# Performance work log

Measured on AMD Instinct MI355X. Metric: run time of the kernel, lower is better.

The kernel has to match this reference:

```python
import jax, jax.numpy as jnp
import numpy as np

TEMPERATURE = 0.07
KNN_AUG = True
NUM_NEIGHBORS = 10
B, N, D = 2048, 65536, 128
NUM_CLUSTERS = 100
EPS = 1e-12


def _l2_normalize(x):
    # matches torch F.normalize(dim=1): x / max(||x||, eps)
    norm = jnp.sqrt(jnp.sum(x * x, axis=1, keepdims=True))
    return x / jnp.maximum(norm, EPS)


def setup_inputs() -> dict:
    key = jax.random.key(0)
    k1, k2, k3, k4 = jax.random.split(key, 4)
    return {
        "features": jax.random.normal(k1, (B, D), dtype=jnp.float32),
        "cluster_idxes": jax.random.randint(k2, (B,), 0, NUM_CLUSTERS),
        "global_features": jax.random.normal(k3, (N, D), dtype=jnp.float32),
        "global_clusters": jax.random.randint(k4, (N,), 0, NUM_CLUSTERS),
    }


def reference(features, cluster_idxes, global_features, global_clusters):
    f = _l2_normalize(features)            # [B, D]
    g = _l2_normalize(global_features)     # [N, D]
    sim = (f @ g.T) / TEMPERATURE          # [B, N]

    # cluster-membership positive mask: [B, N]
    pos_mask = (cluster_idxes[:, None] == global_clusters[None, :]).astype(sim.dtype)

    if KNN_AUG:
        k_val = min(NUM_NEIGHBORS, sim.shape[-1])
        _, knn_idx = jax.lax.top_k(sim, k_val)  # [B, k]
        rows = jnp.arange(sim.shape[0])[:, None]
        knn_mask = jnp.zeros_like(pos_mask).at[rows, knn_idx].set(1.0)
        pos_mask = ((pos_mask + knn_mask) > 0).astype(sim.dtype)

    # masked log-softmax reduction (same math as original: exp/sum/log)
    log_prob = sim - jnp.log(jnp.sum(jnp.exp(sim), axis=1, keepdims=True) + EPS)  # [B, N]
    mean_log_prob_pos = jnp.sum(pos_mask * log_prob, axis=1) / (jnp.sum(pos_mask, axis=1) + EPS)
    return -jnp.mean(mean_log_prob_pos)
```

## Files before the change

### kernel.cpp

```cpp
#include <hip/hip_runtime.h>

#define B_ROWS 2048
#define N_GLB  65536
#define DDIM   128
#define NCLUST 100
#define INV_T  (1.0f/0.07f)
#define LOG2E  1.4426950408889634f
#define LN2    0.6931471805599453f
#define NSPLIT 16
#define CHUNK_COLS (N_GLB/NSPLIT)
#define ITERS (CHUNK_COLS/64)
#define ROWSB 16
#define GRPB 2048
#define TOPK 10
#define CAP  256
#define NSLICE 8
#define TAU_L2E (3.7881f*LOG2E)
#define CSC    65536.0f
#define INV_CSC (1.0f/65536.0f)
#define ZWORDS 105472

typedef __attribute__((ext_vector_type(4))) float f32x4;
typedef __attribute__((ext_vector_type(2))) long lg2;
typedef unsigned long long u64;

__device__ __forceinline__ unsigned fmono(float v) {
  unsigned u = __float_as_uint(v);
  return ((int)u < 0) ? ~u : (u | 0x80000000u);
}
__device__ __forceinline__ float fmono_inv(unsigned m) {
  unsigned u = (m & 0x80000000u) ? (m & 0x7FFFFFFFu) : ~m;
  return __uint_as_float(u);
}
__device__ __forceinline__ u64 mkkey(float val, int col) {
  return ((u64)fmono(val) << 32) | (unsigned)(~(unsigned)col);
}
__device__ __forceinline__ u64 umax64(u64 a, u64 b) { return a > b ? a : b; }

__device__ __forceinline__ float fp8d(unsigned b) {
  unsigned e = (b >> 3) & 15, m = b & 7;
  float v = e ? __uint_as_float(((e + 120u) << 23) | (m << 20))
              : (float)m * 0.001953125f;
  return (b & 0x80u) ? -v : v;
}

__global__ __launch_bounds__(256) void prep_kernel(
    const float* __restrict__ f, const float* __restrict__ g,
    char* __restrict__ wsf2, char* __restrict__ wsg2,
    float* __restrict__ inv_fT, float* __restrict__ inv_g,
    unsigned* __restrict__ zbase) {
  __shared__ unsigned short lds[1024];
  const int t = threadIdx.x, lane = t & 63, w = t >> 6;
  const int grp = blockIdx.x;
  const bool isf = grp < (B_ROWS / 16);

  if (isf) {
    int gid = grp * 256 + t;
    #pragma unroll
    for (int k = 0; k < 4; ++k) {
      int idx = gid + k * 32768;
      if (idx < ZWORDS) zbase[idx] = 0u;
    }
  }

  #pragma unroll
  for (int j = 0; j < 4; ++j) {
    int rit = w * 4 + j;
    int row = grp * 16 + rit;
    int rr = isf ? row : row - B_ROWS;
    const float* src = (isf ? f : g) + (size_t)rr * DDIM;
    float2 v = ((const float2*)src)[lane];
    float ss = v.x * v.x + v.y * v.y;
    #pragma unroll
    for (int m = 32; m; m >>= 1) ss += __shfl_xor(ss, m);
    float inv = 1.0f / fmaxf(sqrtf(ss), 1e-12f);
    if (lane == 0) { if (isf) inv_fT[rr] = inv * INV_T; else inv_g[rr] = inv; }
    float sc = isf ? inv * (INV_T * LOG2E) : inv;
    unsigned pk = __builtin_amdgcn_cvt_pk_fp8_f32(v.x * sc, v.y * sc, 0u, false);
    int k = 2 * lane;
    int off = ((k >> 6) << 10) + (((k >> 3) & 3) << 8) + (rit << 4)
            + (((k >> 5) & 1) << 3) + (k & 7);
    lds[off >> 1] = (unsigned short)(pk & 0xFFFFu);
  }
  __syncthreads();
  char* dst = isf ? (wsf2 + (size_t)grp * GRPB)
                  : (wsg2 + (size_t)(grp - B_ROWS / 16) * GRPB);
  ((uint2*)dst)[t] = ((const uint2*)lds)[t];
}

__global__ __launch_bounds__(256) void csum2_kernel(
    const float* __restrict__ g, const int* __restrict__ gclust,
    const float* __restrict__ inv_g,
    int* __restrict__ csum_i32, int* __restrict__ hist8) {
  __shared__ int cs[NCLUST * DDIM];
  __shared__ int hcnt[NCLUST];
  const int t = threadIdx.x, lane = t & 63, w = t >> 6;
  for (int i = t; i < NCLUST * DDIM; i += 256) cs[i] = 0;
  if (t < NCLUST) hcnt[t] = 0;
  __syncthreads();

  const int rbase = blockIdx.x * 256;
  const int rg = lane >> 4;
  const int ch = lane & 15;
  for (int step = 0; step < 16; ++step) {
    int row = rbase + step * 16 + w * 4 + rg;
    int c = gclust[row];
    float scale = inv_g[row] * CSC;
    const float* gp = g + (size_t)row * DDIM + 8 * ch;
    float4 a = *(const float4*)gp;
    float4 b = *(const float4*)(gp + 4);
    int* dst = &cs[c * DDIM + ch * 8];
    atomicAdd(dst + 0, (int)rintf(a.x * scale));
    atomicAdd(dst + 1, (int)rintf(a.y * scale));
    atomicAdd(dst + 2, (int)rintf(a.z * scale));
    atomicAdd(dst + 3, (int)rintf(a.w * scale));
    atomicAdd(dst + 4, (int)rintf(b.x * scale));
    atomicAdd(dst + 5, (int)rintf(b.y * scale));
    atomicAdd(dst + 6, (int)rintf(b.z * scale));
    atomicAdd(dst + 7, (int)rintf(b.w * scale));
    if (ch == 0) atomicAdd(&hcnt[c], 1);
  }
  __syncthreads();
  const int slice = blockIdx.x & (NSLICE - 1);
  for (int i = t; i < NCLUST * DDIM; i += 256) {
    int x = cs[i];
    if (x) atomicAdd(&csum_i32[(size_t)slice * NCLUST * DDIM + i], x);
  }
  if (t < NCLUST && hcnt[t]) atomicAdd(&hist8[slice * 128 + t], hcnt[t]);
}

#define PUSHQ(av, q)                                                            \
  if ((av) > TAU_L2E) {                                                         \
    int rw = r0 + lhi * 4 + (q);                                                \
    int slot = atomicAdd(&cnt[rw], 1);                                          \
    if (slot < CAP) { lv[rw * CAP + slot] = (av) * LN2; li[rw * CAP + slot] = colv; } \
  }

#define LOADB(dst, gptr)                                                        \
  { dst[0] = *(const uint4*)((gptr) + (size_t)lane * 16);                       \
    dst[1] = *(const uint4*)((gptr) + 1024 + (size_t)lane * 16); }

#define COMPUTE_REFILL(bb, itv, refbase, dorefill)                              \
  {                                                                             \
    f32x4 acA = {0,0,0,0}, acB = {0,0,0,0};                                     \
    lg2 bs0 = __builtin_bit_cast(lg2, bb[0]);                                   \
    lg2 bs1 = __builtin_bit_cast(lg2, bb[1]);                                   \
    if (dorefill) {                                                             \
      bb[0] = *(const uint4*)((refbase) + (size_t)lane * 16);                   \
      bb[1] = *(const uint4*)((refbase) + 1024 + (size_t)lane * 16);            \
    }                                                                           \
    acA = __builtin_amdgcn_mfma_f32_16x16x32_fp8_fp8(afr[0][0], bs0[0], acA, 0, 0, 0); \
    acB = __builtin_amdgcn_mfma_f32_16x16x32_fp8_fp8(afr[1][0], bs1[0], acB, 0, 0, 0); \
    acA = __builtin_amdgcn_mfma_f32_16x16x32_fp8_fp8(afr[0][1], bs0[1], acA, 0, 0, 0); \
    acB = __builtin_amdgcn_mfma_f32_16x16x32_fp8_fp8(afr[1][1], bs1[1], acB, 0, 0, 0); \
    f32x4 a = acA + acB;                                                        \
    se.x += __builtin_amdgcn_exp2f(a.x);                                        \
    se.y += __builtin_amdgcn_exp2f(a.y);                                        \
    se.z += __builtin_amdgcn_exp2f(a.z);                                        \
    se.w += __builtin_amdgcn_exp2f(a.w);                                        \
    float mx = fmaxf(fmaxf(a.x, a.y), fmaxf(a.z, a.w));                         \
    if (mx > TAU_L2E) {                                                         \
      const int colv = chunk * CHUNK_COLS + (itv) * 64 + w * 16 + l15;          \
      PUSHQ(a.x, 0) PUSHQ(a.y, 1) PUSHQ(a.z, 2) PUSHQ(a.w, 3)                   \
    }                                                                           \
  }

__global__ __launch_bounds__(256, 8) void sim_kernel(
    const char* __restrict__ wsf2, const char* __restrict__ wsg2,
    float* __restrict__ p_se, float* __restrict__ lv, int* __restrict__ li,
    int* __restrict__ cnt) {
  __shared__ float sered[4][ROWSB];
  const int t = threadIdx.x, lane = t & 63, w = t >> 6;
  const int l15 = lane & 15, lhi = lane >> 4;
  const int chunk = blockIdx.x;
  const int r0 = blockIdx.y * ROWSB;

  const char* fbase = wsf2 + (size_t)(r0 >> 4) * GRPB;
  lg2 afr[2];
  #pragma unroll
  for (int sp = 0; sp < 2; ++sp)
    afr[sp] = __builtin_bit_cast(lg2,
      *(const uint4*)(fbase + sp * 1024 + (size_t)lane * 16));

  f32x4 se = {0.f, 0.f, 0.f, 0.f};

  const char* gb = wsg2 + (size_t)(chunk * (CHUNK_COLS / 16) + w) * GRPB;
  uint4 b0[2], b1[2];
  LOADB(b0, gb)
  LOADB(b1, gb + 8192)
  for (int it = 0; it < ITERS; it += 2) {
    COMPUTE_REFILL(b0, it,     gb + 2 * 8192, it + 2 < ITERS)
    COMPUTE_REFILL(b1, it + 1, gb + 3 * 8192, it + 3 < ITERS)
    gb += 2 * 8192;
  }

  #pragma unroll
  for (int q = 0; q < 4; ++q) {
    float s = se[q];
    s += __shfl_xor(s, 1); s += __shfl_xor(s, 2);
    s += __shfl_xor(s, 4); s += __shfl_xor(s, 8);
    if (l15 == 0) sered[w][lhi * 4 + q] = s;
  }
  __syncthreads();
  if (t < ROWSB) {
    float s = sered[0][t] + sered[1][t] + sered[2][t] + sered[3][t];
    p_se[(size_t)(r0 + t) * NSPLIT + chunk] = s;
  }
}

__global__ __launch_bounds__(256) void merge_kernel(
    const float* __restrict__ f, const int* __restrict__ fclust,
    const int* __restrict__ gclust, const float* __restrict__ inv_fT,
    const float* __restrict__ p_se, const int* __restrict__ csum_i32,
    const int* __restrict__ hist8, const float* __restrict__ lv,
    const int* __restrict__ li, const int* __restrict__ cnt,
    const char* __restrict__ wsf2, const char* __restrict__ wsg2,
    float* __restrict__ rowv) {
  const int lane = threadIdx.x & 63, w = threadIdx.x >> 6;
  const int r = blockIdx.x * 4 + w;

  float sev = (lane < NSPLIT) ? p_se[(size_t)r * NSPLIT + lane] : 0.f;
  sev += __shfl_xor(sev, 8); sev += __shfl_xor(sev, 4);
  sev += __shfl_xor(sev, 2); sev += __shfl_xor(sev, 1);
  sev = __shfl(sev, 0);

  int rc = fclust[r];
  float2 fv = ((const float2*)(f + (size_t)r * DDIM))[lane];
  float sc = inv_fT[r];
  int ia = 0, ib = 0, hc = 0;
  #pragma unroll
  for (int s = 0; s < NSLICE; ++s) {
    ia += csum_i32[(size_t)s * NCLUST * DDIM + rc * DDIM + 2 * lane];
    ib += csum_i32[(size_t)s * NCLUST * DDIM + rc * DDIM + 2 * lane + 1];
    hc += hist8[s * 128 + rc];
  }
  float dt = fv.x * sc * (ia * INV_CSC) + fv.y * sc * (ib * INV_CSC);
  #pragma unroll
  for (int m = 32; m; m >>= 1) dt += __shfl_xor(dt, m);
  dt = __shfl(dt, 0);

  float Cc = (float)hc;
  int n = cnt[r];
  bool bad = (n < TOPK) || (n > CAP);
  float S10 = 0.f, C10 = 0.f;
  if (!bad) {
    u64 k0 = 0, k1 = 0, k2 = 0, k3 = 0;
    int e = lane;
    if (e < n) k0 = mkkey(lv[(size_t)r * CAP + e], li[(size_t)r * CAP + e]);
    e = lane + 64;
    if (e < n) k1 = mkkey(lv[(size_t)r * CAP + e], li[(size_t)r * CAP + e]);
    e = lane + 128;
    if (e < n) k2 = mkkey(lv[(size_t)r * CAP + e], li[(size_t)r * CAP + e]);
    e = lane + 192;
    if (e < n) k3 = mkkey(lv[(size_t)r * CAP + e], li[(size_t)r * CAP + e]);
    for (int it = 0; it < TOPK; ++it) {
      u64 best = umax64(umax64(k0, k1), umax64(k2, k3));
      #pragma unroll
      for (int m = 32; m; m >>= 1) best = umax64(best, __shfl_xor(best, m));
      float val = fmono_inv((unsigned)(best >> 32));
      int col = (int)(~(unsigned)(best & 0xFFFFFFFFull));
      int gc = gclust[col];
      if (gc != rc) { S10 += val; C10 += 1.f; }
      if (k0 == best) k0 = 0;
      if (k1 == best) k1 = 0;
      if (k2 == best) k2 = 0;
      if (k3 == best) k3 = 0;
    }
  } else {
    uint4 fr[8];
    #pragma unroll
    for (int pc = 0; pc < 8; ++pc)
      fr[pc] = *(const uint4*)(wsf2 + (size_t)(r >> 4) * GRPB + (pc >> 2) * 1024
                               + (pc & 3) * 256 + (r & 15) * 16);
    u64 tk[TOPK];
    #pragma unroll
    for (int i = 0; i < TOPK; ++i) tk[i] = 0;
    for (int col = lane; col < N_GLB; col += 64) {
      const char* gp = wsg2 + (size_t)(col >> 4) * GRPB + (col & 15) * 16;
      float acc = 0.f;
      #pragma unroll
      for (int pc = 0; pc < 8; ++pc) {
        uint4 gv = *(const uint4*)(gp + (pc >> 2) * 1024 + (pc & 3) * 256);
        uint4 fc = fr[pc];
        #pragma unroll
        for (int wd = 0; wd < 4; ++wd) {
          unsigned fa = (&fc.x)[wd], ga = (&gv.x)[wd];
          #pragma unroll
          for (int b = 0; b < 4; ++b)
            acc += fp8d((fa >> (8 * b)) & 0xFFu) * fp8d((ga >> (8 * b)) & 0xFFu);
        }
      }
      u64 key = mkkey(acc, col);
      if (key > tk[0]) {
        u64 cur = key;
        #pragma unroll
        for (int i = 0; i < TOPK - 1; ++i) {
          u64 nxt = tk[i + 1];
          u64 lo = cur < nxt ? cur : nxt;
          u64 hi = cur < nxt ? nxt : cur;
          tk[i] = lo; cur = hi;
        }
        tk[TOPK - 1] = cur;
      }
    }
    for (int it = 0; it < TOPK; ++it) {
      u64 best = tk[TOPK - 1];
      #pragma unroll
      for (int m = 32; m; m >>= 1) best = umax64(best, __shfl_xor(best, m));
      float val = fmono_inv((unsigned)(best >> 32)) * LN2;
      int col = (int)(~(unsigned)(best & 0xFFFFFFFFull));
      if (gclust[col] != rc) { S10 += val; C10 += 1.f; }
      if (tk[TOPK - 1] == best) {
        #pragma unroll
        for (int i = TOPK - 1; i > 0; --i) tk[i] = tk[i - 1];
        tk[0] = 0;
      }
    }
  }
  if (lane == 0) {
    float L = logf(sev + 1e-12f);
    float C = Cc + C10;
    rowv[r] = (dt + S10 - C * L) / (C + 1e-12f);
  }
}

__global__ void final_kernel(const float* __restrict__ rowv, float* __restrict__ out) {
  __shared__ float sm[256];
  int t = threadIdx.x;
  float s = 0.f;
  for (int i = t; i < B_ROWS; i += 256) s += rowv[i];
  sm[t] = s;
  __syncthreads();
  for (int o = 128; o; o >>= 1) { if (t < o) sm[t] += sm[t + o]; __syncthreads(); }
  if (t == 0) out[0] = -(sm[0] / (float)B_ROWS);
}

extern "C" void kernel_launch(void* const* d_in, const int* in_sizes, int n_in,
                              void* d_out, int out_size, void* d_ws, size_t ws_size,
                              hipStream_t stream) {
  const float* f  = (const float*)d_in[0];
  const int*   fc = (const int*)  d_in[1];
  const float* g  = (const float*)d_in[2];
  const int*   gc = (const int*)  d_in[3];
  float* out = (float*)d_out;

  char* ws = (char*)d_ws;
  char*  wsf2    = ws;
  char*  wsg2    = ws + 262144;
  float* inv_fT  = (float*)(ws + 8650752);
  float* inv_g   = (float*)(ws + 8658944);
  float* p_se    = (float*)(ws + 8921088);
  int*   csum_i32= (int*)  (ws + 9052160);
  int*   hist8   = (int*)  (ws + 9461760);
  int*   cnt     = (int*)  (ws + 9465856);
  unsigned* zbase= (unsigned*)(ws + 9052160);
  float* lv      = (float*)(ws + 9474048);
  int*   li      = (int*)  (ws + 11571200);
  float* rowv    = (float*)(ws + 13668352);

  prep_kernel<<<(B_ROWS + N_GLB) / 16, 256, 0, stream>>>(f, g, wsf2, wsg2,
                                                         inv_fT, inv_g, zbase);

  csum2_kernel<<<N_GLB / 256, 256, 0, stream>>>(g, gc, inv_g, csum_i32, hist8);

  dim3 grid(NSPLIT, B_ROWS / ROWSB);
  sim_kernel<<<grid, 256, 0, stream>>>(wsf2, wsg2, p_se, lv, li, cnt);

  merge_kernel<<<B_ROWS / 4, 256, 0, stream>>>(f, fc, gc, inv_fT, p_se, csum_i32,
                                               hist8, lv, li, cnt, wsf2, wsg2, rowv);
  final_kernel<<<1, 256, 0, stream>>>(rowv, out);
}
```

Measured before the change: 106.3 us.

## Fuse global-feature normalization and fp8 packing into cluster-sum kernel

The global-feature normalization and fp8 packing move out of the combined prep kernel into the cluster-sum kernel. The 32 MB g tensor is now read once instead of twice, and the inv_g buffer round-trip goes away. Blocks now cover 128 rows instead of 256, which doubles the block count, and the cluster-sum slices go from 8 to 16 to cut global atomic contention. In exchange there are two block-wide barriers per step for LDS staging, more zeroing work in prepf, and merge reads 16 slices instead of 8.

```diff
diff --git a/kernel.cpp b/kernel.cpp
--- a/kernel.cpp
+++ b/kernel.cpp
@@ -14,11 +14,11 @@
 #define GRPB 2048
 #define TOPK 10
 #define CAP  256
-#define NSLICE 8
+#define NSLICE 16
 #define TAU_L2E (3.7881f*LOG2E)
 #define CSC    65536.0f
 #define INV_CSC (1.0f/65536.0f)
-#define ZWORDS 105472
+#define ZWORDS 208896
 
 typedef __attribute__((ext_vector_type(4))) float f32x4;
 typedef __attribute__((ext_vector_type(2))) long lg2;
@@ -44,20 +44,17 @@
   return (b & 0x80u) ? -v : v;
 }
 
-__global__ __launch_bounds__(256) void prep_kernel(
-    const float* __restrict__ f, const float* __restrict__ g,
-    char* __restrict__ wsf2, char* __restrict__ wsg2,
-    float* __restrict__ inv_fT, float* __restrict__ inv_g,
-    unsigned* __restrict__ zbase) {
+__global__ __launch_bounds__(256) void prepf_kernel(
+    const float* __restrict__ f, char* __restrict__ wsf2,
+    float* __restrict__ inv_fT, unsigned* __restrict__ zbase) {
   __shared__ unsigned short lds[1024];
   const int t = threadIdx.x, lane = t & 63, w = t >> 6;
   const int grp = blockIdx.x;
-  const bool isf = grp < (B_ROWS / 16);
-
-  if (isf) {
+
+  {
     int gid = grp * 256 + t;
     #pragma unroll
-    for (int k = 0; k < 4; ++k) {
+    for (int k = 0; k < 7; ++k) {
       int idx = gid + k * 32768;
       if (idx < ZWORDS) zbase[idx] = 0u;
     }
@@ -66,16 +63,15 @@
   #pragma unroll
   for (int j = 0; j < 4; ++j) {
     int rit = w * 4 + j;
-    int row = grp * 16 + rit;
-    int rr = isf ? row : row - B_ROWS;
-    const float* src = (isf ? f : g) + (size_t)rr * DDIM;
+    int rr = grp * 16 + rit;
+    const float* src = f + (size_t)rr * DDIM;
     float2 v = ((const float2*)src)[lane];
     float ss = v.x * v.x + v.y * v.y;
     #pragma unroll
     for (int m = 32; m; m >>= 1) ss += __shfl_xor(ss, m);
     float inv = 1.0f / fmaxf(sqrtf(ss), 1e-12f);
-    if (lane == 0) { if (isf) inv_fT[rr] = inv * INV_T; else inv_g[rr] = inv; }
-    float sc = isf ? inv * (INV_T * LOG2E) : inv;
+    if (lane == 0) inv_fT[rr] = inv * INV_T;
+    float sc = inv * (INV_T * LOG2E);
     unsigned pk = __builtin_amdgcn_cvt_pk_fp8_f32(v.x * sc, v.y * sc, 0u, false);
     int k = 2 * lane;
     int off = ((k >> 6) << 10) + (((k >> 3) & 3) << 8) + (rit << 4)
@@ -83,32 +79,39 @@
     lds[off >> 1] = (unsigned short)(pk & 0xFFFFu);
   }
   __syncthreads();
-  char* dst = isf ? (wsf2 + (size_t)grp * GRPB)
-                  : (wsg2 + (size_t)(grp - B_ROWS / 16) * GRPB);
-  ((uint2*)dst)[t] = ((const uint2*)lds)[t];
-}
-
-__global__ __launch_bounds__(256) void csum2_kernel(
+  ((uint2*)(wsf2 + (size_t)grp * GRPB))[t] = ((const uint2*)lds)[t];
+}
+
+__global__ __launch_bounds__(256) void prepg_kernel(
     const float* __restrict__ g, const int* __restrict__ gclust,
-    const float* __restrict__ inv_g,
-    int* __restrict__ csum_i32, int* __restrict__ hist8) {
+    char* __restrict__ wsg2,
+    int* __restrict__ csum_i32, int* __restrict__ hist16) {
   __shared__ int cs[NCLUST * DDIM];
   __shared__ int hcnt[NCLUST];
+  __shared__ uint2 stg[256];
   const int t = threadIdx.x, lane = t & 63, w = t >> 6;
+  const int rg = (lane >> 4) & 3;
+  const int ch = lane & 15;
   for (int i = t; i < NCLUST * DDIM; i += 256) cs[i] = 0;
   if (t < NCLUST) hcnt[t] = 0;
   __syncthreads();
 
-  const int rbase = blockIdx.x * 256;
-  const int rg = lane >> 4;
-  const int ch = lane & 15;
-  for (int step = 0; step < 16; ++step) {
+  const int rbase = blockIdx.x * 128;
+  const int soff = ((ch >> 3) << 10) + ((ch & 3) << 8) + ((w * 4 + rg) << 4)
+                 + (((ch >> 2) & 1) << 3);
+
+  for (int step = 0; step < 8; ++step) {
     int row = rbase + step * 16 + w * 4 + rg;
     int c = gclust[row];
-    float scale = inv_g[row] * CSC;
     const float* gp = g + (size_t)row * DDIM + 8 * ch;
     float4 a = *(const float4*)gp;
     float4 b = *(const float4*)(gp + 4);
+    float ss = a.x * a.x + a.y * a.y + a.z * a.z + a.w * a.w
+             + b.x * b.x + b.y * b.y + b.z * b.z + b.w * b.w;
+    ss += __shfl_xor(ss, 1); ss += __shfl_xor(ss, 2);
+    ss += __shfl_xor(ss, 4); ss += __shfl_xor(ss, 8);
+    float inv = 1.0f / fmaxf(sqrtf(ss), 1e-12f);
+    float scale = inv * CSC;
     int* dst = &cs[c * DDIM + ch * 8];
     atomicAdd(dst + 0, (int)rintf(a.x * scale));
     atomicAdd(dst + 1, (int)rintf(a.y * scale));
@@ -119,14 +122,22 @@
     atomicAdd(dst + 6, (int)rintf(b.z * scale));
     atomicAdd(dst + 7, (int)rintf(b.w * scale));
     if (ch == 0) atomicAdd(&hcnt[c], 1);
-  }
-  __syncthreads();
+    unsigned u0 = __builtin_amdgcn_cvt_pk_fp8_f32(a.x * inv, a.y * inv, 0u, false);
+    u0 = __builtin_amdgcn_cvt_pk_fp8_f32(a.z * inv, a.w * inv, u0, true);
+    unsigned u1 = __builtin_amdgcn_cvt_pk_fp8_f32(b.x * inv, b.y * inv, 0u, false);
+    u1 = __builtin_amdgcn_cvt_pk_fp8_f32(b.z * inv, b.w * inv, u1, true);
+    *(uint2*)((char*)stg + soff) = make_uint2(u0, u1);
+    __syncthreads();
+    ((uint2*)(wsg2 + (size_t)(blockIdx.x * 8 + step) * GRPB))[t] = stg[t];
+    __syncthreads();
+  }
+
   const int slice = blockIdx.x & (NSLICE - 1);
   for (int i = t; i < NCLUST * DDIM; i += 256) {
     int x = cs[i];
     if (x) atomicAdd(&csum_i32[(size_t)slice * NCLUST * DDIM + i], x);
   }
-  if (t < NCLUST && hcnt[t]) atomicAdd(&hist8[slice * 128 + t], hcnt[t]);
+  if (t < NCLUST && hcnt[t]) atomicAdd(&hist16[slice * 128 + t], hcnt[t]);
 }
 
 #define PUSHQ(av, q)                                                            \
@@ -212,7 +223,7 @@
     const float* __restrict__ f, const int* __restrict__ fclust,
     const int* __restrict__ gclust, const float* __restrict__ inv_fT,
     const float* __restrict__ p_se, const int* __restrict__ csum_i32,
-    const int* __restrict__ hist8, const float* __restrict__ lv,
+    const int* __restrict__ hist16, const float* __restrict__ lv,
     const int* __restrict__ li, const int* __restrict__ cnt,
     const char* __restrict__ wsf2, const char* __restrict__ wsg2,
     float* __restrict__ rowv) {
@@ -232,7 +243,7 @@
   for (int s = 0; s < NSLICE; ++s) {
     ia += csum_i32[(size_t)s * NCLUST * DDIM + rc * DDIM + 2 * lane];
     ib += csum_i32[(size_t)s * NCLUST * DDIM + rc * DDIM + 2 * lane + 1];
-    hc += hist8[s * 128 + rc];
+    hc += hist16[s * 128 + rc];
   }
   float dt = fv.x * sc * (ia * INV_CSC) + fv.y * sc * (ib * INV_CSC);
   #pragma unroll
@@ -348,25 +359,23 @@
   char*  wsf2    = ws;
   char*  wsg2    = ws + 262144;
   float* inv_fT  = (float*)(ws + 8650752);
-  float* inv_g   = (float*)(ws + 8658944);
-  float* p_se    = (float*)(ws + 8921088);
-  int*   csum_i32= (int*)  (ws + 9052160);
-  int*   hist8   = (int*)  (ws + 9461760);
-  int*   cnt     = (int*)  (ws + 9465856);
-  unsigned* zbase= (unsigned*)(ws + 9052160);
-  float* lv      = (float*)(ws + 9474048);
-  int*   li      = (int*)  (ws + 11571200);
-  float* rowv    = (float*)(ws + 13668352);
-
-  prep_kernel<<<(B_ROWS + N_GLB) / 16, 256, 0, stream>>>(f, g, wsf2, wsg2,
-                                                         inv_fT, inv_g, zbase);
-
-  csum2_kernel<<<N_GLB / 256, 256, 0, stream>>>(g, gc, inv_g, csum_i32, hist8);
+  float* p_se    = (float*)(ws + 8658944);
+  int*   csum_i32= (int*)  (ws + 8790016);
+  int*   hist16  = (int*)  (ws + 9609216);
+  int*   cnt     = (int*)  (ws + 9617408);
+  unsigned* zbase= (unsigned*)(ws + 8790016);
+  float* lv      = (float*)(ws + 9625600);
+  int*   li      = (int*)  (ws + 11722752);
+  float* rowv    = (float*)(ws + 13819904);
+
+  prepf_kernel<<<B_ROWS / 16, 256, 0, stream>>>(f, wsf2, inv_fT, zbase);
+
+  prepg_kernel<<<N_GLB / 128, 256, 0, stream>>>(g, gc, wsg2, csum_i32, hist16);
 
   dim3 grid(NSPLIT, B_ROWS / ROWSB);
   sim_kernel<<<grid, 256, 0, stream>>>(wsf2, wsg2, p_se, lv, li, cnt);
 
   merge_kernel<<<B_ROWS / 4, 256, 0, stream>>>(f, fc, gc, inv_fT, p_se, csum_i32,
-                                               hist8, lv, li, cnt, wsf2, wsg2, rowv);
+                                               hist16, lv, li, cnt, wsf2, wsg2, rowv);
   final_kernel<<<1, 256, 0, stream>>>(rowv, out);
 }
```

Result: slower. 111.3 us (+4.8%).
